# Optimization experiments

Hardware: AMD Instinct MI355X
Metric: run time of the kernel (lower is better)

## Reference

```python
import math
import jax, jax.numpy as jnp
import numpy as np

B, N, D, H = 2, 2048, 1024, 16

def setup_inputs() -> dict:
    key = jax.random.key(0)
    ks = jax.random.split(key, 5)
    x = jax.random.normal(ks[0], (B, N, D), dtype=jnp.float32)
    # causal mask: True = masked (matches masked_fill semantics)
    mask = jnp.broadcast_to(jnp.triu(jnp.ones((N, N), dtype=bool), k=1), (B, N, N))
    sc = 0.02
    Wqkv = jax.random.normal(ks[1], (3 * D, D), dtype=jnp.float32) * sc
    bqkv = jax.random.normal(ks[2], (3 * D,), dtype=jnp.float32) * sc
    Wo = jax.random.normal(ks[3], (D, D), dtype=jnp.float32) * sc
    bo = jax.random.normal(ks[4], (D,), dtype=jnp.float32) * sc
    return {"x": x, "mask": mask, "Wqkv": Wqkv, "bqkv": bqkv, "Wo": Wo, "bo": bo}

def reference(x, mask, Wqkv, bqkv, Wo, bo):
    b, n, d = x.shape
    h = H
    s = d // h
    qkv = x @ Wqkv.T + bqkv                       # [b, n, 3d]
    q, k, v = jnp.split(qkv, 3, axis=2)           # each [b, n, d]
    def heads(z):
        return z.reshape(b, n, h, s).transpose(0, 2, 1, 3)  # [b, h, n, s]
    q, k, v = heads(q), heads(k), heads(v)
    q = q / jnp.asarray(math.sqrt(s), q.dtype)
    a = jnp.einsum('bhqs,bhks->bhqk', q, k)       # [b, h, n, n]
    a = jnp.where(mask[:, None, :, :], -jnp.inf, a)
    a = jax.nn.softmax(a, axis=-1)
    y = jnp.einsum('bhqk,bhks->bhqs', a, v)       # [b, h, n, s]
    y = y.transpose(0, 2, 1, 3).reshape(b, n, d)
    return y @ Wo.T + bo
```

## Files before the change

kernel.cpp:

```cpp
#include <hip/hip_runtime.h>
#include <hip/hip_bf16.h>
#include <stdint.h>

#define BB 2
#define NN 2048
#define DD 1024
#define HH 16
#define SS 64

typedef short short8 __attribute__((ext_vector_type(8)));
typedef float f32x4 __attribute__((ext_vector_type(4)));

__device__ __forceinline__ float bf2f(uint16_t u) {
    return __uint_as_float(((uint32_t)u) << 16);
}
__device__ __forceinline__ uint16_t f2bf(float f) {
    uint32_t u = __float_as_uint(f);
    return (uint16_t)((u + 0x7FFFu + ((u >> 16) & 1u)) >> 16);
}
__device__ __forceinline__ short8 cvt8(float4 a, float4 b) {
    short8 s;
    s[0] = (short)f2bf(a.x); s[1] = (short)f2bf(a.y);
    s[2] = (short)f2bf(a.z); s[3] = (short)f2bf(a.w);
    s[4] = (short)f2bf(b.x); s[5] = (short)f2bf(b.y);
    s[6] = (short)f2bf(b.z); s[7] = (short)f2bf(b.w);
    return s;
}

__device__ __forceinline__ void load_lds16(const uint16_t* g, uint16_t* l) {
    __builtin_amdgcn_global_load_lds(
        (const __attribute__((address_space(1))) void*)g,
        (__attribute__((address_space(3))) void*)l, 16, 0, 0);
}

#define XE  (4096 * 1024)
#define WQE (3072 * 1024)
#define WOE (1024 * 1024)

__global__ __launch_bounds__(256) void cvt_all(
    const float* __restrict__ x, const float* __restrict__ wq,
    const float* __restrict__ wo, uint16_t* __restrict__ dst)
{
    int i = (blockIdx.x * 256 + threadIdx.x) * 8;
    const float* src;
    int off;
    if (i < XE)            { src = x;  off = i; }
    else if (i < XE + WQE) { src = wq; off = i - XE; }
    else                   { src = wo; off = i - XE - WQE; }
    float4 a = *(const float4*)(src + off);
    float4 b = *(const float4*)(src + off + 4);
    *(short8*)(dst + i) = cvt8(a, b);
}

__global__ __launch_bounds__(256) void gemm_qkv(
    const uint16_t* __restrict__ X, const uint16_t* __restrict__ W,
    const float* __restrict__ bias,
    uint16_t* __restrict__ Qb, uint16_t* __restrict__ Kb, uint16_t* __restrict__ Vt)
{
    __shared__ __align__(16) uint16_t smem[18432];
    uint16_t* As = smem;
    uint16_t* Bs = smem + 4096;

    const int tid = threadIdx.x;
    const int w = tid >> 6, l = tid & 63;
    const int lq = l & 15, lg = l >> 4;
    const int wm = w >> 1, wn = w & 1;
    const int m0 = blockIdx.y * 128;
    const int n0 = blockIdx.x * 128;

    f32x4 acc[4][4] = {};

    for (int k0 = 0; k0 < 1024; k0 += 32) {
        __syncthreads();
        #pragma unroll
        for (int j = 0; j < 2; ++j) {
            const int c = (j * 4 + w) * 64 + l;
            load_lds16(X + (size_t)(m0 + (c >> 2)) * 1024 + k0 + (c & 3) * 8,
                       As + (j * 4 + w) * 512);
            load_lds16(W + (size_t)(n0 + (c >> 2)) * 1024 + k0 + (c & 3) * 8,
                       Bs + (j * 4 + w) * 512);
        }
        __syncthreads();
        short8 af[4], bfr[4];
        #pragma unroll
        for (int mi = 0; mi < 4; ++mi)
            af[mi] = *(const short8*)&As[(wm * 64 + mi * 16 + lq) * 32 + lg * 8];
        #pragma unroll
        for (int ni = 0; ni < 4; ++ni)
            bfr[ni] = *(const short8*)&Bs[(wn * 64 + ni * 16 + lq) * 32 + lg * 8];
        #pragma unroll
        for (int mi = 0; mi < 4; ++mi)
            #pragma unroll
            for (int ni = 0; ni < 4; ++ni)
                acc[mi][ni] = __builtin_amdgcn_mfma_f32_16x16x32_bf16(
                    af[mi], bfr[ni], acc[mi][ni], 0, 0, 0);
    }

    __syncthreads();
    const int part = n0 >> 10;
    const int hh = ((n0 + wn * 64) & 1023) >> 6;
    const int mrow0 = m0 + wm * 64;
    const int bh = (mrow0 >> 11) * 16 + hh;
    const int tok0 = mrow0 & 2047;
    const float scl = (part == 0) ? 0.125f * 1.44269504089f : 1.0f;

    float bias4[4];
    #pragma unroll
    for (int ni = 0; ni < 4; ++ni)
        bias4[ni] = bias[n0 + wn * 64 + ni * 16 + lq];

    uint16_t* T = smem + w * 4608;
    if (part < 2) {
        #pragma unroll
        for (int mi = 0; mi < 4; ++mi)
            #pragma unroll
            for (int ni = 0; ni < 4; ++ni)
                #pragma unroll
                for (int r = 0; r < 4; ++r)
                    T[(mi * 16 + lg * 4 + r) * 72 + ni * 16 + lq] =
                        f2bf((acc[mi][ni][r] + bias4[ni]) * scl);
    } else {
        #pragma unroll
        for (int mi = 0; mi < 4; ++mi)
            #pragma unroll
            for (int ni = 0; ni < 4; ++ni)
                #pragma unroll
                for (int r = 0; r < 4; ++r)
                    T[(ni * 16 + lq) * 72 + mi * 16 + lg * 4 + r] =
                        f2bf(acc[mi][ni][r] + bias4[ni]);
    }

    const int a0 = l >> 3, b8 = (l & 7) * 8;
    #pragma unroll
    for (int i = 0; i < 8; ++i) {
        int a = i * 8 + a0;
        short8 u = *(short8*)&T[a * 72 + b8];
        uint16_t* p;
        if (part < 2) {
            uint16_t* dst = (part == 0) ? Qb : Kb;
            p = dst + ((size_t)bh * 2048 + tok0 + a) * 64 + b8;
        } else {
            p = Vt + ((size_t)bh * 64 + a) * 2048 + tok0 + b8;
        }
        *(short8*)p = u;
    }
}

__device__ __forceinline__ void loadKf(const uint16_t* Kb, int kv0, int lq, int lg,
                                       short8 (&d)[8]) {
    #pragma unroll
    for (int n = 0; n < 4; ++n) {
        const uint16_t* kb = Kb + (size_t)(kv0 + n * 16 + lq) * 64 + lg * 8;
        d[2 * n]     = *(const short8*)kb;
        d[2 * n + 1] = *(const short8*)(kb + 32);
    }
}
__device__ __forceinline__ void loadVf(const uint16_t* Vb, int kv0, int lq, int lg,
                                       short8 (&d)[8]) {
    #pragma unroll
    for (int n = 0; n < 4; ++n) {
        const uint16_t* vb = Vb + (size_t)(n * 16 + lq) * 2048 + kv0 + lg * 8;
        d[2 * n]     = *(const short8*)vb;
        d[2 * n + 1] = *(const short8*)(vb + 32);
    }
}

#define DEFER_THR 11.5f

__global__ __launch_bounds__(64) void attn_mfma(
    const uint16_t* __restrict__ Q, const uint16_t* __restrict__ K,
    const uint16_t* __restrict__ Vt, uint16_t* __restrict__ Y)
{
    const int id = blockIdx.x;
    const int bh = id & 31;
    const int blk = 63 - (id >> 5);
    const int qt = blk >> 1;
    const int q0 = blk * 32;

    const int lane = threadIdx.x;
    const int lq = lane & 15;
    const int lg = lane >> 4;

    __shared__ __align__(16) uint16_t Pl[2][16][72];

    const uint16_t* Kb = K + (size_t)bh * (2048 * 64);
    const uint16_t* Vb = Vt + (size_t)bh * (64 * 2048);
    const int b = bh >> 4, h = bh & 15;

    short8 qf[2][2];
    #pragma unroll
    for (int sub = 0; sub < 2; ++sub) {
        const uint16_t* qb = Q + ((size_t)bh * 2048 + q0 + sub * 16 + lq) * 64 + lg * 8;
        qf[sub][0] = *(const short8*)qb;
        qf[sub][1] = *(const short8*)(qb + 32);
    }

    f32x4 y[2][4] = {};
    float m[2]    = {-INFINITY, -INFINITY};
    float lsum[2] = {0.f, 0.f};

    short8 kf[8], vv[8];
    loadKf(Kb, 0, lq, lg, kf);

    for (int kt = 0; kt <= qt; ++kt) {
        const int kv0 = kt * 64;
        loadVf(Vb, kv0, lq, lg, vv);

        f32x4 z[2][4];
        __builtin_amdgcn_s_setprio(1);
        #pragma unroll
        for (int sub = 0; sub < 2; ++sub)
            #pragma unroll
            for (int n = 0; n < 4; ++n) {
                f32x4 t = {};
                t = __builtin_amdgcn_mfma_f32_16x16x32_bf16(kf[2 * n], qf[sub][0], t, 0, 0, 0);
                z[sub][n] = __builtin_amdgcn_mfma_f32_16x16x32_bf16(kf[2 * n + 1], qf[sub][1], t, 0, 0, 0);
            }
        __builtin_amdgcn_s_setprio(0);

        if (kt < qt) loadKf(Kb, kv0 + 64, lq, lg, kf);

        #pragma unroll
        for (int sub = 0; sub < 2; ++sub) {
            if (kt == qt) {
                const int qrow = q0 + sub * 16 + lq;
                #pragma unroll
                for (int n = 0; n < 4; ++n) {
                    const int kvb = kv0 + n * 16 + lg * 4;
                    #pragma unroll
                    for (int r = 0; r < 4; ++r)
                        if (kvb + r > qrow) z[sub][n][r] = -INFINITY;
                }
            }
            float mt = -INFINITY;
            #pragma unroll
            for (int n = 0; n < 4; ++n)
                #pragma unroll
                for (int r = 0; r < 4; ++r)
                    mt = fmaxf(mt, z[sub][n][r]);
            const bool skip = __all(mt - m[sub] <= DEFER_THR);

            if (!skip) {
                float mf = fmaxf(mt, __shfl_xor(mt, 16));
                mf = fmaxf(mf, __shfl_xor(mf, 32));
                const float mn = fmaxf(m[sub], mf);
                const float sc = exp2f(m[sub] - mn);
                m[sub] = mn;
                lsum[sub] *= sc;
                float scy[4];
                #pragma unroll
                for (int r = 0; r < 4; ++r) scy[r] = __shfl(sc, lg * 4 + r);
                #pragma unroll
                for (int n = 0; n < 4; ++n)
                    #pragma unroll
                    for (int r = 0; r < 4; ++r)
                        y[sub][n][r] *= scy[r];
            }

            float ps = 0.f;
            uint32_t pk0[4], pk1[4];
            #pragma unroll
            for (int n = 0; n < 4; ++n) {
                float e0 = exp2f(z[sub][n][0] - m[sub]);
                float e1 = exp2f(z[sub][n][1] - m[sub]);
                float e2 = exp2f(z[sub][n][2] - m[sub]);
                float e3 = exp2f(z[sub][n][3] - m[sub]);
                ps += (e0 + e1) + (e2 + e3);
                asm("v_cvt_pk_bf16_f32 %0, %1, %2" : "=v"(pk0[n]) : "v"(e0), "v"(e1));
                asm("v_cvt_pk_bf16_f32 %0, %1, %2" : "=v"(pk1[n]) : "v"(e2), "v"(e3));
            }
            lsum[sub] += ps;
            #pragma unroll
            for (int n = 0; n < 4; ++n) {
                uint2 u; u.x = pk0[n]; u.y = pk1[n];
                *(uint2*)&Pl[sub][lq][n * 16 + lg * 4] = u;
            }

            short8 pa0 = *(short8*)&Pl[sub][lq][lg * 8];
            short8 pa1 = *(short8*)&Pl[sub][lq][lg * 8 + 32];
            __builtin_amdgcn_s_setprio(1);
            #pragma unroll
            for (int n = 0; n < 4; ++n) {
                y[sub][n] = __builtin_amdgcn_mfma_f32_16x16x32_bf16(pa0, vv[2 * n], y[sub][n], 0, 0, 0);
                y[sub][n] = __builtin_amdgcn_mfma_f32_16x16x32_bf16(pa1, vv[2 * n + 1], y[sub][n], 0, 0, 0);
            }
            __builtin_amdgcn_s_setprio(0);
        }
    }

    #pragma unroll
    for (int sub = 0; sub < 2; ++sub) {
        float ls = lsum[sub];
        ls += __shfl_xor(ls, 16);
        ls += __shfl_xor(ls, 32);
        const float inv = 1.0f / ls;
        float invy[4];
        #pragma unroll
        for (int r = 0; r < 4; ++r) invy[r] = __shfl(inv, lg * 4 + r);
        #pragma unroll
        for (int r = 0; r < 4; ++r) {
            int token = b * 2048 + q0 + sub * 16 + lg * 4 + r;
            uint16_t* yrow = Y + (size_t)token * 1024 + h * 64;
            #pragma unroll
            for (int n = 0; n < 4; ++n)
                yrow[n * 16 + lq] = f2bf(y[sub][n][r] * invy[r]);
        }
    }
}

__global__ __launch_bounds__(256) void gemm_proj(
    const uint16_t* __restrict__ Yin, const uint16_t* __restrict__ W,
    const float* __restrict__ bias, float* __restrict__ out)
{
    __shared__ __align__(16) uint16_t smem[8192];
    uint16_t* As = smem;
    uint16_t* Bs = smem + 4096;

    const int tid = threadIdx.x;
    const int w = tid >> 6, l = tid & 63;
    const int lq = l & 15, lg = l >> 4;
    const int wm = w >> 1, wn = w & 1;
    const int m0 = blockIdx.y * 128;
    const int n0 = blockIdx.x * 128;

    f32x4 acc[4][4] = {};

    for (int k0 = 0; k0 < 1024; k0 += 32) {
        __syncthreads();
        #pragma unroll
        for (int j = 0; j < 2; ++j) {
            const int c = (j * 4 + w) * 64 + l;
            load_lds16(Yin + (size_t)(m0 + (c >> 2)) * 1024 + k0 + (c & 3) * 8,
                       As + (j * 4 + w) * 512);
            load_lds16(W + (size_t)(n0 + (c >> 2)) * 1024 + k0 + (c & 3) * 8,
                       Bs + (j * 4 + w) * 512);
        }
        __syncthreads();
        short8 af[4], bfr[4];
        #pragma unroll
        for (int mi = 0; mi < 4; ++mi)
            af[mi] = *(const short8*)&As[(wm * 64 + mi * 16 + lq) * 32 + lg * 8];
        #pragma unroll
        for (int ni = 0; ni < 4; ++ni)
            bfr[ni] = *(const short8*)&Bs[(wn * 64 + ni * 16 + lq) * 32 + lg * 8];
        #pragma unroll
        for (int mi = 0; mi < 4; ++mi)
            #pragma unroll
            for (int ni = 0; ni < 4; ++ni)
                acc[mi][ni] = __builtin_amdgcn_mfma_f32_16x16x32_bf16(
                    af[mi], bfr[ni], acc[mi][ni], 0, 0, 0);
    }

    const int mrow0 = m0 + wm * 64;
    const int ncol0 = n0 + wn * 64;
    float bias4[4];
    #pragma unroll
    for (int ni = 0; ni < 4; ++ni)
        bias4[ni] = bias[ncol0 + ni * 16 + lq];

    #pragma unroll
    for (int mi = 0; mi < 4; ++mi)
        #pragma unroll
        for (int r = 0; r < 4; ++r) {
            const size_t rowoff = (size_t)(mrow0 + mi * 16 + lg * 4 + r) * 1024;
            #pragma unroll
            for (int ni = 0; ni < 4; ++ni)
                out[rowoff + ncol0 + ni * 16 + lq] = acc[mi][ni][r] + bias4[ni];
        }
}


extern "C" void kernel_launch(void* const* d_in, const int* in_sizes, int n_in,
                              void* d_out, int out_size, void* d_ws, size_t ws_size,
                              hipStream_t stream) {
    const float* x    = (const float*)d_in[0];
    const float* Wqkv = (const float*)d_in[2];
    const float* bqkv = (const float*)d_in[3];
    const float* Wo   = (const float*)d_in[4];
    const float* bo   = (const float*)d_in[5];

    const size_t QK = (size_t)BB * HH * NN * SS;

    uint16_t* Xb  = (uint16_t*)d_ws;
    uint16_t* Wqb = Xb + XE;
    uint16_t* Wob = Wqb + WQE;
    uint16_t* Qb  = Wob + WOE;
    uint16_t* Kb  = Qb + QK;
    uint16_t* Vt  = Kb + QK;
    uint16_t* Yb  = Vt + QK;

    cvt_all<<<(XE + WQE + WOE) / 8 / 256, 256, 0, stream>>>(x, Wqkv, Wo, Xb);
    gemm_qkv<<<dim3(24, 32), 256, 0, stream>>>(Xb, Wqb, bqkv, Qb, Kb, Vt);
    attn_mfma<<<2048, 64, 0, stream>>>(Qb, Kb, Vt, Yb);
    gemm_proj<<<dim3(8, 32), 256, 0, stream>>>(Yb, Wob, bo, (float*)d_out);
}
```

Before: 153.5 us.

## Split attention KV loop across two waves with shared-memory softmax merge

```diff
diff --git a/kernel.cpp b/kernel.cpp
--- a/kernel.cpp
+++ b/kernel.cpp
@@ -167,7 +167,7 @@
 
 #define DEFER_THR 11.5f
 
-__global__ __launch_bounds__(64) void attn_mfma(
+__global__ __launch_bounds__(128) void attn_mfma(
     const uint16_t* __restrict__ Q, const uint16_t* __restrict__ K,
     const uint16_t* __restrict__ Vt, uint16_t* __restrict__ Y)
 {
@@ -177,11 +177,14 @@
     const int qt = blk >> 1;
     const int q0 = blk * 32;
 
-    const int lane = threadIdx.x;
+    const int wv = threadIdx.x >> 6;
+    const int lane = threadIdx.x & 63;
     const int lq = lane & 15;
     const int lg = lane >> 4;
 
-    __shared__ __align__(16) uint16_t Pl[2][16][72];
+    __shared__ __align__(16) uint16_t Pl[2][2][16][72];
+    __shared__ float  My[32][68];
+    __shared__ float2 Mml[32];
 
     const uint16_t* Kb = K + (size_t)bh * (2048 * 64);
     const uint16_t* Vb = Vt + (size_t)bh * (64 * 2048);
@@ -200,9 +203,9 @@
     float lsum[2] = {0.f, 0.f};
 
     short8 kf[8], vv[8];
-    loadKf(Kb, 0, lq, lg, kf);
-
-    for (int kt = 0; kt <= qt; ++kt) {
+    loadKf(Kb, wv * 64, lq, lg, kf);
+
+    for (int kt = wv; kt <= qt; kt += 2) {
         const int kv0 = kt * 64;
         loadVf(Vb, kv0, lq, lg, vv);
 
@@ -218,7 +221,7 @@
             }
         __builtin_amdgcn_s_setprio(0);
 
-        if (kt < qt) loadKf(Kb, kv0 + 64, lq, lg, kf);
+        if (kt + 2 <= qt) loadKf(Kb, kv0 + 128, lq, lg, kf);
 
         #pragma unroll
         for (int sub = 0; sub < 2; ++sub) {
@@ -273,11 +276,11 @@
             #pragma unroll
             for (int n = 0; n < 4; ++n) {
                 uint2 u; u.x = pk0[n]; u.y = pk1[n];
-                *(uint2*)&Pl[sub][lq][n * 16 + lg * 4] = u;
-            }
-
-            short8 pa0 = *(short8*)&Pl[sub][lq][lg * 8];
-            short8 pa1 = *(short8*)&Pl[sub][lq][lg * 8 + 32];
+                *(uint2*)&Pl[wv][sub][lq][n * 16 + lg * 4] = u;
+            }
+
+            short8 pa0 = *(short8*)&Pl[wv][sub][lq][lg * 8];
+            short8 pa1 = *(short8*)&Pl[wv][sub][lq][lg * 8 + 32];
             __builtin_amdgcn_s_setprio(1);
             #pragma unroll
             for (int n = 0; n < 4; ++n) {
@@ -288,22 +291,54 @@
         }
     }
 
+    float ls[2];
     #pragma unroll
     for (int sub = 0; sub < 2; ++sub) {
-        float ls = lsum[sub];
-        ls += __shfl_xor(ls, 16);
-        ls += __shfl_xor(ls, 32);
-        const float inv = 1.0f / ls;
-        float invy[4];
-        #pragma unroll
-        for (int r = 0; r < 4; ++r) invy[r] = __shfl(inv, lg * 4 + r);
-        #pragma unroll
-        for (int r = 0; r < 4; ++r) {
-            int token = b * 2048 + q0 + sub * 16 + lg * 4 + r;
-            uint16_t* yrow = Y + (size_t)token * 1024 + h * 64;
+        float t = lsum[sub];
+        t += __shfl_xor(t, 16);
+        t += __shfl_xor(t, 32);
+        ls[sub] = t;
+    }
+
+    if (wv == 1) {
+        #pragma unroll
+        for (int sub = 0; sub < 2; ++sub) {
             #pragma unroll
             for (int n = 0; n < 4; ++n)
-                yrow[n * 16 + lq] = f2bf(y[sub][n][r] * invy[r]);
+                #pragma unroll
+                for (int r = 0; r < 4; ++r)
+                    My[sub * 16 + lg * 4 + r][n * 16 + lq] = y[sub][n][r];
+            if (lg == 0) Mml[sub * 16 + lq] = make_float2(m[sub], ls[sub]);
+        }
+    }
+    __syncthreads();
+    if (wv == 0) {
+        #pragma unroll
+        for (int sub = 0; sub < 2; ++sub) {
+            float2 o = Mml[sub * 16 + lq];
+            const float m1 = o.x, l1 = o.y;
+            const float mx = fmaxf(m[sub], m1);
+            const float w0 = exp2f(m[sub] - mx);
+            const float w1 = exp2f(m1 - mx);
+            const float inv = 1.0f / (ls[sub] * w0 + l1 * w1);
+            const float f0 = w0 * inv, f1 = w1 * inv;
+            float f0r[4], f1r[4];
+            #pragma unroll
+            for (int r = 0; r < 4; ++r) {
+                f0r[r] = __shfl(f0, lg * 4 + r);
+                f1r[r] = __shfl(f1, lg * 4 + r);
+            }
+            #pragma unroll
+            for (int r = 0; r < 4; ++r) {
+                int token = b * 2048 + q0 + sub * 16 + lg * 4 + r;
+                uint16_t* yrow = Y + (size_t)token * 1024 + h * 64;
+                #pragma unroll
+                for (int n = 0; n < 4; ++n) {
+                    float val = y[sub][n][r] * f0r[r] +
+                                My[sub * 16 + lg * 4 + r][n * 16 + lq] * f1r[r];
+                    yrow[n * 16 + lq] = f2bf(val);
+                }
+            }
         }
     }
 }
@@ -391,6 +426,6 @@
 
     cvt_all<<<(XE + WQE + WOE) / 8 / 256, 256, 0, stream>>>(x, Wqkv, Wo, Xb);
     gemm_qkv<<<dim3(24, 32), 256, 0, stream>>>(Xb, Wqb, bqkv, Qb, Kb, Vt);
-    attn_mfma<<<2048, 64, 0, stream>>>(Qb, Kb, Vt, Yb);
+    attn_mfma<<<2048, 128, 0, stream>>>(Qb, Kb, Vt, Yb);
     gemm_proj<<<dim3(8, 32), 256, 0, stream>>>(Yb, Wob, bo, (float*)d_out);
 }
```

After: 149.9 us. 1.02x faster.
